# Optimization experiments

Measured on AMD Instinct MI355X. Metric: run time of the kernel, lower is better.

## Reference

```python
import jax, jax.numpy as jnp
import numpy as np

NEG_INF = -1e10  # matches the -10000000000.0 additive mask in the torch source


def setup_inputs() -> dict:
    key = jax.random.key(0)
    k1, k2, k3, k4 = jax.random.split(key, 4)
    bs, h, S, d = 4, 16, 2048, 64
    bs_h = bs * h
    query = jax.random.normal(k1, (bs_h, S, d), dtype=jnp.float32)
    key_t = jax.random.normal(k2, (bs_h, S, d), dtype=jnp.float32)
    value = jax.random.normal(k3, (bs_h, S, d), dtype=jnp.float32)
    attn_mask = jax.random.randint(k4, (bs, S), 0, 2).astype(jnp.int32)
    return {"query": query, "key": key_t, "value": value,
            "attn_mask": attn_mask, "decod_mask": 1}


def reference(query, key, value, attn_mask, decod_mask):
    bs_h, K, d_k = key.shape
    Q = query.shape[1]
    bs = attn_mask.shape[0]
    h = bs_h // bs

    # scores: [bs_h, Q, K]
    scores = jnp.einsum('bqd,bkd->bqk', query, key) / jnp.sqrt(
        jnp.asarray(d_k, dtype=query.dtype))

    # padding mask: positions where attn_mask == 0 get -1e10.
    # torch repeats the [bs, Q, K] mask h times along the batch axis
    # (order: [mask; mask; ...]), i.e. batch index b in bs_h maps to b % bs.
    pad = (attn_mask == 0).astype(scores.dtype) * NEG_INF  # [bs, K]
    scores = (scores.reshape(h, bs, Q, K) + pad[None, :, None, :]).reshape(bs_h, Q, K)

    if decod_mask is not None:
        causal = jnp.triu(jnp.full((Q, K), NEG_INF, dtype=scores.dtype), k=1)
        scores = scores + causal[None, :, :]

    attn = jax.nn.softmax(scores, axis=-1)
    # dropout p=0.0 -> identity
    return jnp.einsum('bqk,bkd->bqd', attn, value)
```

## Files before the change

### kernel.cpp

```cpp
#include <hip/hip_runtime.h>
#include <hip/hip_bf16.h>

#define S_LEN 2048
#define DH 64
#define NBATCH 4
#define LOG2E 1.44269504088896f
#define SCL2E 0.18033688011112042f
#define PADC  (-1.44269504088896e10f)
#define NEG_BIG -1e10f
#define NEG_CAUSAL -3.0e38f

typedef __attribute__((ext_vector_type(8))) short short8;
typedef __attribute__((ext_vector_type(4))) float floatx4;
typedef __attribute__((ext_vector_type(4))) unsigned uintx4;

__device__ inline float fast_exp2(float x) {
#if __has_builtin(__builtin_amdgcn_exp2f)
  return __builtin_amdgcn_exp2f(x);
#else
  return exp2f(x);
#endif
}

__device__ inline short f2bf(float x) {
  union { float f; unsigned u; } v; v.f = x;
  unsigned r = v.u + 0x7fffu + ((v.u >> 16) & 1u);
  return (short)(r >> 16);
}

__device__ inline short8 pack8(float4 a, float4 b) {
  short8 r;
  r[0] = f2bf(a.x); r[1] = f2bf(a.y); r[2] = f2bf(a.z); r[3] = f2bf(a.w);
  r[4] = f2bf(b.x); r[5] = f2bf(b.y); r[6] = f2bf(b.z); r[7] = f2bf(b.w);
  return r;
}

__device__ inline float4 scale4(float4 v, float m) {
  return make_float4(v.x * m, v.y * m, v.z * m, v.w * m);
}

__device__ inline unsigned packhi(unsigned hi, unsigned lo) {
#if __has_builtin(__builtin_amdgcn_perm)
  return __builtin_amdgcn_perm(hi, lo, 0x07060302u);
#else
  return (hi & 0xFFFF0000u) | (lo >> 16);
#endif
}

#define MFMA32(a, b, c) __builtin_amdgcn_mfma_f32_16x16x32_bf16(a, b, c, 0, 0, 0)

__global__ void prep_aux2(const int* __restrict__ maskg,
                          unsigned long long* __restrict__ mb,
                          int* __restrict__ fn)
{
  const int b = (int)blockIdx.x;
  const int tid = (int)threadIdx.x;
  __shared__ int sF[4], sN[4];

  if (tid < 32) {
    const int* mp = &maskg[b * S_LEN + tid * 64];
    unsigned long long m = 0ull;
#pragma unroll
    for (int j = 0; j < 64; j += 4) {
      int4 v = *(const int4*)&mp[j];
      unsigned nib = (v.x ? 1u : 0u) | (v.y ? 2u : 0u) | (v.z ? 4u : 0u) | (v.w ? 8u : 0u);
      m |= (unsigned long long)nib << j;
    }
    mb[b * 32 + tid] = m;
  }

  int fmin = S_LEN, n = 0;
  for (int k = tid; k < S_LEN; k += 256)
    if (maskg[b * S_LEN + k] != 0) { ++n; if (k < fmin) fmin = k; }
#pragma unroll
  for (int off = 1; off < 64; off <<= 1) {
    fmin = min(fmin, __shfl_xor(fmin, off));
    n += __shfl_xor(n, off);
  }
  const int w = tid >> 6;
  if ((tid & 63) == 0) { sF[w] = fmin; sN[w] = n; }
  __syncthreads();
  if (tid == 0) {
    int F = sF[0], N = sN[0];
#pragma unroll
    for (int i = 1; i < 4; ++i) { F = min(F, sF[i]); N += sN[i]; }
    fn[b * 2] = F; fn[b * 2 + 1] = N;
  }
}

#define KT_STRIDE 72
#define SR_STRIDE 68

__global__ __launch_bounds__(256, 2) void prep_kv2(
    const float* __restrict__ Kg, const float* __restrict__ Vg,
    const int* __restrict__ maskg,
    short8* __restrict__ Kf, short8* __restrict__ Vf,
    float* __restrict__ sums)
{
  const int blk = (int)blockIdx.x;
  const int bh = blk >> 5, kt = blk & 31;
  const int b = bh & (NBATCH - 1);
  const int tid = (int)threadIdx.x;
  const int row = tid >> 2, seg = tid & 3;

  __shared__ __align__(16) short Kt[64 * KT_STRIDE];
  __shared__ __align__(16) short Vt[64 * KT_STRIDE];
  __shared__ __align__(16) float sredf[64 * SR_STRIDE];

  const size_t gbase = ((size_t)bh * S_LEN + kt * 64 + row) * DH + seg * 16;
  {
    float4 a0 = *(const float4*)(Kg + gbase);
    float4 a1 = *(const float4*)(Kg + gbase + 4);
    float4 a2 = *(const float4*)(Kg + gbase + 8);
    float4 a3 = *(const float4*)(Kg + gbase + 12);
    *(short8*)&Kt[row * KT_STRIDE + seg * 16]     = pack8(a0, a1);
    *(short8*)&Kt[row * KT_STRIDE + seg * 16 + 8] = pack8(a2, a3);
  }
  {
    float4 a0 = *(const float4*)(Vg + gbase);
    float4 a1 = *(const float4*)(Vg + gbase + 4);
    float4 a2 = *(const float4*)(Vg + gbase + 8);
    float4 a3 = *(const float4*)(Vg + gbase + 12);
    *(short8*)&Vt[row * KT_STRIDE + seg * 16]     = pack8(a0, a1);
    *(short8*)&Vt[row * KT_STRIDE + seg * 16 + 8] = pack8(a2, a3);
    const float mf = (maskg[b * S_LEN + kt * 64 + row] != 0) ? 1.f : 0.f;
    float* sr = &sredf[row * SR_STRIDE + seg * 16];
    *(float4*)(sr + 0)  = scale4(a0, mf);
    *(float4*)(sr + 4)  = scale4(a1, mf);
    *(float4*)(sr + 8)  = scale4(a2, mf);
    *(float4*)(sr + 12) = scale4(a3, mf);
  }
  __syncthreads();

  const int w = tid >> 6, lane = tid & 63;
  const int c = lane & 15, g = lane >> 4;
  const size_t obase = (size_t)(bh * 32 + kt) * 8;

#pragma unroll
  for (int i = 0; i < 2; ++i) {
    const int q = 2 * w + i;
    const int ks = q >> 2, nt = q & 3;
    short8 v = *(const short8*)&Kt[(nt * 16 + c) * KT_STRIDE + ks * 32 + g * 8];
    Kf[(obase + q) * 64 + lane] = v;
  }
#pragma unroll
  for (int i = 0; i < 2; ++i) {
    const int q = 2 * w + i;
    const int nt2 = q >> 2, dt = q & 3;
    short8 r;
#pragma unroll
    for (int j = 0; j < 8; ++j) {
      const int key = nt2 * 32 + ((j >= 4) ? 16 : 0) + g * 4 + (j & 3);
      r[j] = Vt[key * KT_STRIDE + dt * 16 + c];
    }
    Vf[(obase + q) * 64 + lane] = r;
  }
  if (tid < 64) {
    float a = 0.f;
#pragma unroll 8
    for (int r2 = 0; r2 < 64; ++r2) a += sredf[r2 * SR_STRIDE + tid];
    atomicAdd(&sums[bh * 64 + tid], a);
  }
}

__device__ __forceinline__ void loadk(const short8* __restrict__ kbase, int kt,
                                      int lane, short8 (&dst)[8]) {
  const short8* p = kbase + ((size_t)kt * 8) * 64 + lane;
#pragma unroll
  for (int i = 0; i < 8; ++i) dst[i] = p[i * 64];
}

__device__ __forceinline__ void loadv(const short8* __restrict__ vbase, int kt,
                                      int lane, short8 (&dst)[8]) {
  const short8* p = vbase + ((size_t)kt * 8) * 64 + lane;
#pragma unroll
  for (int i = 0; i < 8; ++i) dst[i] = p[i * 64];
}

__device__ __forceinline__ void compute_tile(
    int kt, int qbase, int c, int g,
    const short8 (&kf)[8], unsigned long long mb, const short8 (&vf)[8],
    const short8 (&qf)[2][2], const short8& ones,
    floatx4 (&acc)[2][4], floatx4 (&acc_l)[2])
{
  const unsigned long long sh = mb >> (g * 4);
  const unsigned mlo = (unsigned)sh, mhi = (unsigned)(sh >> 32);
  floatx4 padv[4];
#pragma unroll
  for (int r = 0; r < 4; ++r) {
    padv[0][r] = ((mlo >> r) & 1u)        ? 0.f : PADC;
    padv[1][r] = ((mlo >> (16 + r)) & 1u) ? 0.f : PADC;
    padv[2][r] = ((mhi >> r) & 1u)        ? 0.f : PADC;
    padv[3][r] = ((mhi >> (16 + r)) & 1u) ? 0.f : PADC;
  }

#pragma unroll
  for (int s2 = 0; s2 < 2; ++s2) {
    if (kt * 64 > qbase + s2 * 16 + 15) continue;
    floatx4 st[4];
    __builtin_amdgcn_s_setprio(1);
#pragma unroll
    for (int nt = 0; nt < 4; ++nt) {
      floatx4 cc = (floatx4){0.f, 0.f, 0.f, 0.f};
      cc = MFMA32(kf[nt],     qf[s2][0], cc);
      cc = MFMA32(kf[4 + nt], qf[s2][1], cc);
      st[nt] = cc;
    }
    __builtin_amdgcn_s_setprio(0);
    const int q = qbase + s2 * 16 + c;
    const bool causal = (kt * 64 + 63) > (qbase + s2 * 16);
    unsigned pu[4][4];
#pragma unroll
    for (int nt = 0; nt < 4; ++nt) {
#pragma unroll
      for (int r = 0; r < 4; ++r) {
        float arg = fmaf(st[nt][r], SCL2E, padv[nt][r]);
        if (causal) {
          const int key = kt * 64 + nt * 16 + g * 4 + r;
          arg = (key > q) ? NEG_CAUSAL : arg;
        }
        pu[nt][r] = __float_as_uint(fast_exp2(arg)) + 0x8000u;
      }
    }
    short8 pP[2];
#pragma unroll
    for (int nt2 = 0; nt2 < 2; ++nt2) {
      uintx4 wv;
      wv[0] = packhi(pu[2 * nt2][1],     pu[2 * nt2][0]);
      wv[1] = packhi(pu[2 * nt2][3],     pu[2 * nt2][2]);
      wv[2] = packhi(pu[2 * nt2 + 1][1], pu[2 * nt2 + 1][0]);
      wv[3] = packhi(pu[2 * nt2 + 1][3], pu[2 * nt2 + 1][2]);
      pP[nt2] = __builtin_bit_cast(short8, wv);
    }
    __builtin_amdgcn_s_setprio(1);
#pragma unroll
    for (int nt2 = 0; nt2 < 2; ++nt2) {
      acc_l[s2] = MFMA32(pP[nt2], ones, acc_l[s2]);
#pragma unroll
      for (int dt = 0; dt < 4; ++dt)
        acc[s2][dt] = MFMA32(pP[nt2], vf[nt2 * 4 + dt], acc[s2][dt]);
    }
    __builtin_amdgcn_s_setprio(0);
  }
}

__global__ __launch_bounds__(256, 2) void flash_fwd7(
    const float* __restrict__ Qg,
    const unsigned long long* __restrict__ mbArr,
    const short8* __restrict__ KfB, const short8* __restrict__ VfB,
    float* __restrict__ Og)
{
  const int bh = blockIdx.x;
  const int b  = bh & (NBATCH - 1);
  const int tid = (int)threadIdx.x;
  const int w = tid >> 6, lane = tid & 63;
  const int widx = (int)blockIdx.y * 4 + w;
  const int c = lane & 15, g = lane >> 4;

  const short8 ones = {0x3F80, 0x3F80, 0x3F80, 0x3F80, 0x3F80, 0x3F80, 0x3F80, 0x3F80};
  const short8* kbase = KfB + (size_t)bh * 32 * 8 * 64;
  const short8* vbase = VfB + (size_t)bh * 32 * 8 * 64;

#pragma unroll
  for (int half = 0; half < 2; ++half) {
    const int ch = half ? (63 - widx) : widx;
    const int qbase = ch * 32;
    const int ktmax = ch >> 1;

    short8 qf[2][2];
#pragma unroll
    for (int s2 = 0; s2 < 2; ++s2) {
      const float* qp = Qg + ((size_t)bh * S_LEN + qbase + s2 * 16 + c) * DH + g * 8;
#pragma unroll
      for (int ks = 0; ks < 2; ++ks) {
        float4 a  = *(const float4*)(qp + ks * 32);
        float4 b4 = *(const float4*)(qp + ks * 32 + 4);
        qf[s2][ks] = pack8(a, b4);
      }
    }

    floatx4 acc[2][4];
    floatx4 acc_l[2];
#pragma unroll
    for (int s2 = 0; s2 < 2; ++s2) {
      acc_l[s2] = (floatx4){0.f, 0.f, 0.f, 0.f};
#pragma unroll
      for (int dt = 0; dt < 4; ++dt) acc[s2][dt] = (floatx4){0.f, 0.f, 0.f, 0.f};
    }

    short8 kfA[8], kfB_[8];
    unsigned long long mbA = mbArr[(b << 5)];
    unsigned long long mbB = 0ull;
    loadk(kbase, 0, lane, kfA);
    for (int kt = 0; kt <= ktmax; kt += 2) {
      const bool hasB = (kt + 1 <= ktmax);
      {
        short8 vf[8];
        loadv(vbase, kt, lane, vf);
        if (hasB) {
          loadk(kbase, kt + 1, lane, kfB_);
          mbB = mbArr[(b << 5) | (kt + 1)];
        }
        compute_tile(kt, qbase, c, g, kfA, mbA, vf, qf, ones, acc, acc_l);
      }
      if (hasB) {
        short8 vf[8];
        loadv(vbase, kt + 1, lane, vf);
        if (kt + 2 <= ktmax) {
          loadk(kbase, kt + 2, lane, kfA);
          mbA = mbArr[(b << 5) | (kt + 2)];
        }
        compute_tile(kt + 1, qbase, c, g, kfB_, mbB, vf, qf, ones, acc, acc_l);
      }
    }

#pragma unroll
    for (int s2 = 0; s2 < 2; ++s2) {
      float rr[4];
#pragma unroll
      for (int r = 0; r < 4; ++r) rr[r] = 1.f / acc_l[s2][r];
#pragma unroll
      for (int dt = 0; dt < 4; ++dt)
#pragma unroll
        for (int r = 0; r < 4; ++r)
          Og[((size_t)bh * S_LEN + qbase + s2 * 16 + g * 4 + r) * DH + dt * 16 + c] =
              acc[s2][dt][r] * rr[r];
    }
  }
}

__global__ void fixup_write2(const float* __restrict__ Vg, const int* __restrict__ fn,
                             const float* __restrict__ sums, float* __restrict__ Og)
{
  const int bh = blockIdx.x;
  const int b  = bh & (NBATCH - 1);
  const int d  = (int)threadIdx.x;
  const int f  = fn[b * 2], n = fn[b * 2 + 1];
  if (f == 0) return;
  const float ms = sums[bh * 64 + d];
  float pre = 0.f;
  for (int q = 0; q < f; ++q) {
    pre += Vg[((size_t)bh * S_LEN + q) * DH + d];
    Og[((size_t)bh * S_LEN + q) * DH + d] = (pre + ms) / (float)(q + 1 + n);
  }
}

__global__ __launch_bounds__(256, 2) void flash_fwd_lds(
    const float* __restrict__ Qg, const float* __restrict__ Kg,
    const float* __restrict__ Vg, const int* __restrict__ maskg,
    float* __restrict__ Og)
{
  const int qt  = blockIdx.x;
  const int bh  = blockIdx.y;
  const int b   = bh & (NBATCH - 1);
  const int tid = (int)threadIdx.x;
  const int w = tid >> 6, lane = tid & 63;
  const int g = lane >> 4, c = lane & 15;

  __shared__ __align__(16) short Ks[64 * 72];
  __shared__ __align__(16) short Vt[64 * 72];
  __shared__ __align__(16) short Ps[4][32 * 72];

  short8 qf[2][2];
#pragma unroll
  for (int s2 = 0; s2 < 2; ++s2) {
    const float* qp = Qg + ((size_t)bh * S_LEN + qt * 128 + w * 32 + s2 * 16 + c) * DH + g * 8;
#pragma unroll
    for (int ks = 0; ks < 2; ++ks) {
      float4 a  = *(const float4*)(qp + ks * 32);
      float4 bq = *(const float4*)(qp + ks * 32 + 4);
      qf[s2][ks] = pack8(a, bq);
    }
  }

  floatx4 acc[2][4];
  float mrow[2][4], lrow[2][4];
#pragma unroll
  for (int s2 = 0; s2 < 2; ++s2) {
#pragma unroll
    for (int i = 0; i < 4; ++i) acc[s2][i] = (floatx4){0.f, 0.f, 0.f, 0.f};
#pragma unroll
    for (int r = 0; r < 4; ++r) { mrow[s2][r] = -3.4e38f; lrow[s2][r] = 0.f; }
  }

  const int rstage = tid >> 2;
  const int dstage = (tid & 3) * 16;
  const int ktmax = 2 * qt + 1;

  for (int kt = 0; kt <= ktmax; ++kt) {
    __syncthreads();
    {
      const size_t rowbase = ((size_t)bh * S_LEN + kt * 64 + rstage) * DH + dstage;
      const float* kp = Kg + rowbase;
      const float* vp = Vg + rowbase;
      float4 k0 = *(const float4*)kp;       float4 k1 = *(const float4*)(kp + 4);
      float4 k2 = *(const float4*)(kp + 8); float4 k3 = *(const float4*)(kp + 12);
      *(short8*)&Ks[rstage * 72 + dstage]     = pack8(k0, k1);
      *(short8*)&Ks[rstage * 72 + dstage + 8] = pack8(k2, k3);
      float4 v0 = *(const float4*)vp;       float4 v1 = *(const float4*)(vp + 4);
      float4 v2 = *(const float4*)(vp + 8); float4 v3 = *(const float4*)(vp + 12);
      float vv[16] = {v0.x, v0.y, v0.z, v0.w, v1.x, v1.y, v1.z, v1.w,
                      v2.x, v2.y, v2.z, v2.w, v3.x, v3.y, v3.z, v3.w};
#pragma unroll
      for (int i = 0; i < 16; ++i) Vt[(dstage + i) * 72 + rstage] = f2bf(vv[i]);
    }
    __syncthreads();

    float padv[4];
#pragma unroll
    for (int nt = 0; nt < 4; ++nt)
      padv[nt] = (maskg[b * S_LEN + kt * 64 + nt * 16 + c] != 0) ? 0.f : NEG_BIG;

    short8 kf[2][4];
#pragma unroll
    for (int ks = 0; ks < 2; ++ks)
#pragma unroll
      for (int nt = 0; nt < 4; ++nt)
        kf[ks][nt] = *(const short8*)&Ks[(nt * 16 + c) * 72 + ks * 32 + g * 8];

    bool act[2];
#pragma unroll
    for (int s2 = 0; s2 < 2; ++s2)
      act[s2] = (kt * 64) <= (qt * 128 + w * 32 + s2 * 16 + 15);

#pragma unroll
    for (int s2 = 0; s2 < 2; ++s2) {
      if (!act[s2]) continue;
      floatx4 sv[4];
#pragma unroll
      for (int nt = 0; nt < 4; ++nt) {
        floatx4 cc = (floatx4){0.f, 0.f, 0.f, 0.f};
        cc = MFMA32(qf[s2][0], kf[0][nt], cc);
        cc = MFMA32(qf[s2][1], kf[1][nt], cc);
        sv[nt] = cc;
      }
      const int qrow0 = qt * 128 + w * 32 + s2 * 16 + g * 4;
#pragma unroll
      for (int nt = 0; nt < 4; ++nt) {
        const int key = kt * 64 + nt * 16 + c;
#pragma unroll
        for (int r = 0; r < 4; ++r) {
          float s = sv[nt][r] * 0.125f + padv[nt];
          if (key > qrow0 + r) s = NEG_CAUSAL;
          sv[nt][r] = s;
        }
      }
#pragma unroll
      for (int r = 0; r < 4; ++r) {
        float mx = fmaxf(fmaxf(sv[0][r], sv[1][r]), fmaxf(sv[2][r], sv[3][r]));
        mx = fmaxf(mx, __shfl_xor(mx, 1));
        mx = fmaxf(mx, __shfl_xor(mx, 2));
        mx = fmaxf(mx, __shfl_xor(mx, 4));
        mx = fmaxf(mx, __shfl_xor(mx, 8));
        const float mold = mrow[s2][r];
        const float mnew = fmaxf(mold, mx);
        const float corr = fast_exp2((mold - mnew) * LOG2E);
        float ps = 0.f;
#pragma unroll
        for (int nt = 0; nt < 4; ++nt) {
          float p = fast_exp2((sv[nt][r] - mnew) * LOG2E);
          sv[nt][r] = p;
          ps += p;
        }
        ps += __shfl_xor(ps, 1);
        ps += __shfl_xor(ps, 2);
        ps += __shfl_xor(ps, 4);
        ps += __shfl_xor(ps, 8);
        lrow[s2][r] = lrow[s2][r] * corr + ps;
        mrow[s2][r] = mnew;
#pragma unroll
        for (int dt = 0; dt < 4; ++dt) acc[s2][dt][r] *= corr;
      }
#pragma unroll
      for (int nt = 0; nt < 4; ++nt)
#pragma unroll
        for (int r = 0; r < 4; ++r)
          Ps[w][(s2 * 16 + g * 4 + r) * 72 + nt * 16 + c] = f2bf(sv[nt][r]);
    }

#pragma unroll
    for (int ks = 0; ks < 2; ++ks) {
      short8 pf0 = {}, pf1 = {};
      if (act[0]) pf0 = *(const short8*)&Ps[w][c * 72 + ks * 32 + g * 8];
      if (act[1]) pf1 = *(const short8*)&Ps[w][(16 + c) * 72 + ks * 32 + g * 8];
#pragma unroll
      for (int dt = 0; dt < 4; ++dt) {
        short8 vfr = *(const short8*)&Vt[(dt * 16 + c) * 72 + ks * 32 + g * 8];
        if (act[0]) acc[0][dt] = MFMA32(pf0, vfr, acc[0][dt]);
        if (act[1]) acc[1][dt] = MFMA32(pf1, vfr, acc[1][dt]);
      }
    }
  }

#pragma unroll
  for (int s2 = 0; s2 < 2; ++s2) {
    float rl[4];
#pragma unroll
    for (int r = 0; r < 4; ++r) rl[r] = 1.f / lrow[s2][r];
    const size_t obase = ((size_t)bh * S_LEN + qt * 128 + w * 32 + s2 * 16 + g * 4) * DH + c;
#pragma unroll
    for (int dt = 0; dt < 4; ++dt)
#pragma unroll
      for (int r = 0; r < 4; ++r)
        Og[obase + (size_t)r * DH + dt * 16] = acc[s2][dt][r] * rl[r];
  }
}

__global__ void fixup(const float* __restrict__ Vg, const int* __restrict__ maskg,
                      float* __restrict__ Og)
{
  const int bh = blockIdx.x;
  const int b  = bh & (NBATCH - 1);
  const int tid = (int)threadIdx.x;
  __shared__ int sFirst;
  __shared__ float4 sRed[64][16];
  __shared__ int sCnt[64];
  if (tid == 0) sFirst = S_LEN;
  __syncthreads();
  for (int k = tid; k < S_LEN; k += 1024)
    if (maskg[b * S_LEN + k] != 0) atomicMin(&sFirst, k);
  __syncthreads();
  const int f = sFirst;
  if (f == 0) return;

  const int dq = tid & 15, kg = tid >> 4;
  float4 a = {0.f, 0.f, 0.f, 0.f}; int cnt = 0;
  for (int k = kg; k < S_LEN; k += 64) {
    if (maskg[b * S_LEN + k] != 0) {
      float4 v = *(const float4*)&Vg[((size_t)bh * S_LEN + k) * DH + dq * 4];
      a.x += v.x; a.y += v.y; a.z += v.z; a.w += v.w; cnt++;
    }
  }
  sRed[kg][dq] = a;
  if (dq == 0) sCnt[kg] = cnt;
  __syncthreads();
  if (tid < 64) {
    const int q4 = tid >> 2, e = tid & 3;
    float ms = 0.f; int n = 0;
#pragma unroll 4
    for (int i = 0; i < 64; ++i) {
      const float* p4 = (const float*)&sRed[i][q4];
      ms += p4[e];
      n += sCnt[i];
    }
    float pre = 0.f;
    for (int q = 0; q < f; ++q) {
      pre += Vg[((size_t)bh * S_LEN + q) * DH + tid];
      Og[((size_t)bh * S_LEN + q) * DH + tid] = (pre + ms) / (float)(q + 1 + n);
    }
  }
}

extern "C" void kernel_launch(void* const* d_in, const int* in_sizes, int n_in,
                              void* d_out, int out_size, void* d_ws, size_t ws_size,
                              hipStream_t stream) {
  const float* Q = (const float*)d_in[0];
  const float* K = (const float*)d_in[1];
  const float* V = (const float*)d_in[2];
  const int* mask = (const int*)d_in[3];
  float* O = (float*)d_out;

  const size_t KF_BYTES  = (size_t)64 * S_LEN * DH * 2;
  const size_t SUM_BYTES = (size_t)4096 * sizeof(float);
  const size_t MB_BYTES  = (size_t)128 * sizeof(unsigned long long);
  const size_t FN_BYTES  = (size_t)8 * sizeof(int);
  if (ws_size >= 2 * KF_BYTES + SUM_BYTES + MB_BYTES + FN_BYTES) {
    short8* Kf = (short8*)d_ws;
    short8* Vf = (short8*)((char*)d_ws + KF_BYTES);
    float* sums = (float*)((char*)d_ws + 2 * KF_BYTES);
    unsigned long long* mbArr =
        (unsigned long long*)((char*)d_ws + 2 * KF_BYTES + SUM_BYTES);
    int* fn = (int*)((char*)d_ws + 2 * KF_BYTES + SUM_BYTES + MB_BYTES);
    hipMemsetAsync(sums, 0, SUM_BYTES, stream);
    prep_aux2<<<dim3(4), dim3(256), 0, stream>>>(mask, mbArr, fn);
    prep_kv2<<<dim3(2048), dim3(256), 0, stream>>>(K, V, mask, Kf, Vf, sums);
    flash_fwd7<<<dim3(64, 8), dim3(256), 0, stream>>>(Q, mbArr, Kf, Vf, O);
    fixup_write2<<<dim3(64), dim3(64), 0, stream>>>(V, fn, sums, O);
  } else {
    flash_fwd_lds<<<dim3(16, 64), dim3(256), 0, stream>>>(Q, K, V, mask, O);
    fixup<<<dim3(64), dim3(1024), 0, stream>>>(V, mask, O);
  }
}
```

Before: 203.7 us.

## Fuse mask prep and fixup into main kernels, replace atomics with partial sums

Folds the mask-bitmap construction into the K/V prep kernel using a wave ballot, and drops the separate aux kernel and the memset. Per-tile masked V column sums are now written as partials instead of being accumulated with atomics. The fully-masked-prefix fixup moves into the tail of the flash kernel, where it recomputes the first-valid index and count from the bitmap. The goal is fewer launches and less serialisation. In exchange, the masked sums are taken from bf16-rounded V rather than fp32, and every wave redundantly rescans the bitmap and the partial sums.

```diff
diff --git a/kernel.cpp b/kernel.cpp
--- a/kernel.cpp
+++ b/kernel.cpp
@@ -35,10 +35,6 @@
   return r;
 }
 
-__device__ inline float4 scale4(float4 v, float m) {
-  return make_float4(v.x * m, v.y * m, v.z * m, v.w * m);
-}
-
 __device__ inline unsigned packhi(unsigned hi, unsigned lo) {
 #if __has_builtin(__builtin_amdgcn_perm)
   return __builtin_amdgcn_perm(hi, lo, 0x07060302u);
@@ -49,53 +45,13 @@
 
 #define MFMA32(a, b, c) __builtin_amdgcn_mfma_f32_16x16x32_bf16(a, b, c, 0, 0, 0)
 
-__global__ void prep_aux2(const int* __restrict__ maskg,
-                          unsigned long long* __restrict__ mb,
-                          int* __restrict__ fn)
-{
-  const int b = (int)blockIdx.x;
-  const int tid = (int)threadIdx.x;
-  __shared__ int sF[4], sN[4];
-
-  if (tid < 32) {
-    const int* mp = &maskg[b * S_LEN + tid * 64];
-    unsigned long long m = 0ull;
-#pragma unroll
-    for (int j = 0; j < 64; j += 4) {
-      int4 v = *(const int4*)&mp[j];
-      unsigned nib = (v.x ? 1u : 0u) | (v.y ? 2u : 0u) | (v.z ? 4u : 0u) | (v.w ? 8u : 0u);
-      m |= (unsigned long long)nib << j;
-    }
-    mb[b * 32 + tid] = m;
-  }
-
-  int fmin = S_LEN, n = 0;
-  for (int k = tid; k < S_LEN; k += 256)
-    if (maskg[b * S_LEN + k] != 0) { ++n; if (k < fmin) fmin = k; }
-#pragma unroll
-  for (int off = 1; off < 64; off <<= 1) {
-    fmin = min(fmin, __shfl_xor(fmin, off));
-    n += __shfl_xor(n, off);
-  }
-  const int w = tid >> 6;
-  if ((tid & 63) == 0) { sF[w] = fmin; sN[w] = n; }
-  __syncthreads();
-  if (tid == 0) {
-    int F = sF[0], N = sN[0];
-#pragma unroll
-    for (int i = 1; i < 4; ++i) { F = min(F, sF[i]); N += sN[i]; }
-    fn[b * 2] = F; fn[b * 2 + 1] = N;
-  }
-}
-
 #define KT_STRIDE 72
-#define SR_STRIDE 68
-
-__global__ __launch_bounds__(256, 2) void prep_kv2(
+
+__global__ __launch_bounds__(256, 2) void prep3(
     const float* __restrict__ Kg, const float* __restrict__ Vg,
     const int* __restrict__ maskg,
     short8* __restrict__ Kf, short8* __restrict__ Vf,
-    float* __restrict__ sums)
+    unsigned long long* __restrict__ mb, float* __restrict__ psum)
 {
   const int blk = (int)blockIdx.x;
   const int bh = blk >> 5, kt = blk & 31;
@@ -105,7 +61,6 @@
 
   __shared__ __align__(16) short Kt[64 * KT_STRIDE];
   __shared__ __align__(16) short Vt[64 * KT_STRIDE];
-  __shared__ __align__(16) float sredf[64 * SR_STRIDE];
 
   const size_t gbase = ((size_t)bh * S_LEN + kt * 64 + row) * DH + seg * 16;
   {
@@ -123,12 +78,6 @@
     float4 a3 = *(const float4*)(Vg + gbase + 12);
     *(short8*)&Vt[row * KT_STRIDE + seg * 16]     = pack8(a0, a1);
     *(short8*)&Vt[row * KT_STRIDE + seg * 16 + 8] = pack8(a2, a3);
-    const float mf = (maskg[b * S_LEN + kt * 64 + row] != 0) ? 1.f : 0.f;
-    float* sr = &sredf[row * SR_STRIDE + seg * 16];
-    *(float4*)(sr + 0)  = scale4(a0, mf);
-    *(float4*)(sr + 4)  = scale4(a1, mf);
-    *(float4*)(sr + 8)  = scale4(a2, mf);
-    *(float4*)(sr + 12) = scale4(a3, mf);
   }
   __syncthreads();
 
@@ -155,11 +104,19 @@
     }
     Vf[(obase + q) * 64 + lane] = r;
   }
+
   if (tid < 64) {
-    float a = 0.f;
-#pragma unroll 8
-    for (int r2 = 0; r2 < 64; ++r2) a += sredf[r2 * SR_STRIDE + tid];
-    atomicAdd(&sums[bh * 64 + tid], a);
+    const unsigned long long wm =
+        __ballot(maskg[b * S_LEN + kt * 64 + tid] != 0);
+    if (bh < NBATCH && tid == 0) mb[bh * 32 + kt] = wm;
+    float s = 0.f;
+#pragma unroll 4
+    for (int r2 = 0; r2 < 64; ++r2) {
+      const float m = ((wm >> r2) & 1ull) ? 1.f : 0.f;
+      const unsigned bits = (unsigned)(unsigned short)Vt[r2 * KT_STRIDE + tid];
+      s = fmaf(m, __uint_as_float(bits << 16), s);
+    }
+    psum[(size_t)(bh * 32 + kt) * 64 + tid] = s;
   }
 }
 
@@ -244,9 +201,10 @@
   }
 }
 
-__global__ __launch_bounds__(256, 2) void flash_fwd7(
-    const float* __restrict__ Qg,
+__global__ __launch_bounds__(256, 2) void flash_fwd8(
+    const float* __restrict__ Qg, const float* __restrict__ Vg,
     const unsigned long long* __restrict__ mbArr,
+    const float* __restrict__ psum,
     const short8* __restrict__ KfB, const short8* __restrict__ VfB,
     float* __restrict__ Og)
 {
@@ -327,21 +285,35 @@
               acc[s2][dt][r] * rr[r];
     }
   }
-}
-
-__global__ void fixup_write2(const float* __restrict__ Vg, const int* __restrict__ fn,
-                             const float* __restrict__ sums, float* __restrict__ Og)
-{
-  const int bh = blockIdx.x;
-  const int b  = bh & (NBATCH - 1);
-  const int d  = (int)threadIdx.x;
-  const int f  = fn[b * 2], n = fn[b * 2 + 1];
-  if (f == 0) return;
-  const float ms = sums[bh * 64 + d];
-  float pre = 0.f;
-  for (int q = 0; q < f; ++q) {
-    pre += Vg[((size_t)bh * S_LEN + q) * DH + d];
-    Og[((size_t)bh * S_LEN + q) * DH + d] = (pre + ms) / (float)(q + 1 + n);
+
+  {
+    int f = S_LEN, n = 0;
+#pragma unroll 4
+    for (int kt = 0; kt < 32; ++kt) {
+      const unsigned long long m = mbArr[(b << 5) | kt];
+      n += __popcll(m);
+      if (f == S_LEN && m != 0ull) f = kt * 64 + (__ffsll((long long)m) - 1);
+    }
+    if (f > 0) {
+#pragma unroll
+      for (int half = 0; half < 2; ++half) {
+        const int ch = half ? (63 - widx) : widx;
+        const int qb = ch * 32;
+        if (qb >= f) continue;
+        float ms = 0.f;
+#pragma unroll 4
+        for (int kt = 0; kt < 32; ++kt)
+          ms += psum[(size_t)(bh * 32 + kt) * 64 + lane];
+        const int qend = min(f, qb + 32);
+        float pre = 0.f;
+        for (int q = 0; q < qend; ++q) {
+          pre += Vg[((size_t)bh * S_LEN + q) * DH + lane];
+          if (q >= qb)
+            Og[((size_t)bh * S_LEN + q) * DH + lane] =
+                (pre + ms) / (float)(q + 1 + n);
+        }
+      }
+    }
   }
 }
 
@@ -560,22 +532,17 @@
   const int* mask = (const int*)d_in[3];
   float* O = (float*)d_out;
 
-  const size_t KF_BYTES  = (size_t)64 * S_LEN * DH * 2;
-  const size_t SUM_BYTES = (size_t)4096 * sizeof(float);
-  const size_t MB_BYTES  = (size_t)128 * sizeof(unsigned long long);
-  const size_t FN_BYTES  = (size_t)8 * sizeof(int);
-  if (ws_size >= 2 * KF_BYTES + SUM_BYTES + MB_BYTES + FN_BYTES) {
+  const size_t KF_BYTES   = (size_t)64 * S_LEN * DH * 2;
+  const size_t PSUM_BYTES = (size_t)64 * 32 * 64 * sizeof(float);
+  const size_t MB_BYTES   = (size_t)128 * sizeof(unsigned long long);
+  if (ws_size >= 2 * KF_BYTES + PSUM_BYTES + MB_BYTES) {
     short8* Kf = (short8*)d_ws;
     short8* Vf = (short8*)((char*)d_ws + KF_BYTES);
-    float* sums = (float*)((char*)d_ws + 2 * KF_BYTES);
+    float* psum = (float*)((char*)d_ws + 2 * KF_BYTES);
     unsigned long long* mbArr =
-        (unsigned long long*)((char*)d_ws + 2 * KF_BYTES + SUM_BYTES);
-    int* fn = (int*)((char*)d_ws + 2 * KF_BYTES + SUM_BYTES + MB_BYTES);
-    hipMemsetAsync(sums, 0, SUM_BYTES, stream);
-    prep_aux2<<<dim3(4), dim3(256), 0, stream>>>(mask, mbArr, fn);
-    prep_kv2<<<dim3(2048), dim3(256), 0, stream>>>(K, V, mask, Kf, Vf, sums);
-    flash_fwd7<<<dim3(64, 8), dim3(256), 0, stream>>>(Q, mbArr, Kf, Vf, O);
-    fixup_write2<<<dim3(64), dim3(64), 0, stream>>>(V, fn, sums, O);
+        (unsigned long long*)((char*)d_ws + 2 * KF_BYTES + PSUM_BYTES);
+    prep3<<<dim3(2048), dim3(256), 0, stream>>>(K, V, mask, Kf, Vf, mbArr, psum);
+    flash_fwd8<<<dim3(64, 8), dim3(256), 0, stream>>>(Q, V, mbArr, psum, Kf, Vf, O);
   } else {
     flash_fwd_lds<<<dim3(16, 64), dim3(256), 0, stream>>>(Q, K, V, mask, O);
     fixup<<<dim3(64), dim3(1024), 0, stream>>>(V, mask, O);
```

New measurement: 198.6 us. -2.5%, faster.
